# Kernel optimization log

Measured on AMD Instinct MI355X. Metric: run time of the kernel, lower is better.

The kernel has to match this reference:

```python
import jax, jax.numpy as jnp
import numpy as np

N, K, CONV_DIM = 100, 20, 256
TEMP, ALPHA = 0.1, 0.1
B_NORM = 1  # module hardcodes self.B = 1
BATCH = 8


def setup_inputs() -> dict:
    key = jax.random.key(0)
    inputs = jax.random.normal(key, (BATCH, N, K, CONV_DIM), dtype=jnp.float32)
    return {"inputs": inputs}


def reference(inputs) -> jnp.ndarray:
    # inputs: [B, N, K, D] prototype representations
    B, n, k, D = inputs.shape
    # L2-normalize along feature dim (reduce_euclidean_norm)
    xn = inputs / jnp.sqrt(jnp.sum(inputs * inputs, axis=-1, keepdims=True))
    flat = xn.reshape(B, n * k, D)  # all prototypes, all classes: [B, N*K, D]

    # anchor-vs-all similarities: [B, N, K, N*K]
    sims = jnp.einsum('bnkd,bmd->bnkm', xn, flat) / TEMP
    # anchor self-similarity (==1/t after normalization, but keep exact math): [B, N, K]
    self_sim = jnp.sum(xn * xn, axis=-1) / TEMP

    # denominator: sum_m exp(sim) - exp(self)
    denom = jnp.sum(jnp.exp(sims), axis=-1) - jnp.exp(self_sim)
    log_term = jnp.log(denom)  # [B, N, K]

    # intra-class similarity sum: anchor vs all K prototypes of its own class
    intra = jnp.einsum('bnkd,bnjd->bnk', xn, xn) / TEMP  # [B, N, K]
    sum_term = (intra - self_sim) / (k - 1)

    cl_loss = jnp.sum(log_term - sum_term)  # summed over batch and all N*K anchors
    loss = ALPHA * cl_loss / (B_NORM * n * k * D)
    return loss
```

## Files before the change

### kernel.cpp

```cpp
#include <hip/hip_runtime.h>
#include <math.h>

#define BB 8
#define NN 100
#define KK 20
#define DD 256
#define MM 2000
#define MP 2048
#define TINV 10.0f
#define LOSS_SCALE 1.953125e-7f

typedef __bf16 bf16x8 __attribute__((ext_vector_type(8)));
typedef float floatx4 __attribute__((ext_vector_type(4)));
typedef __attribute__((address_space(1))) const ushort GUshort;
typedef __attribute__((address_space(3))) ushort LUshort;

__device__ __forceinline__ ushort f2bf(float f) {
    unsigned int u = __float_as_uint(f);
    u += 0x7fffu + ((u >> 16) & 1u);
    return (ushort)(u >> 16);
}

__global__ void norm_bf16(const float* __restrict__ x, ushort* __restrict__ xb,
                          float* __restrict__ invn_out,
                          float* __restrict__ denom_g, float* __restrict__ out) {
    if (blockIdx.x < 16)
        ((float4*)denom_g)[blockIdx.x * 256 + threadIdx.x] = make_float4(0.f, 0.f, 0.f, 0.f);
    if (blockIdx.x == 0 && threadIdx.x == 0) out[0] = 0.0f;

    const int rg = blockIdx.x * 4 + (threadIdx.x >> 6);
    const int lane = threadIdx.x & 63;
    const int b = rg >> 11;
    const int r = rg & (MP - 1);
    ushort4 outv = make_ushort4(0, 0, 0, 0);
    if (r < MM) {
        const float4 v = ((const float4*)(x + ((size_t)(b * MM + r)) * DD))[lane];
        float s = v.x * v.x + v.y * v.y + v.z * v.z + v.w * v.w;
        #pragma unroll
        for (int o = 32; o >= 1; o >>= 1) s += __shfl_xor(s, o, 64);
        const float inv = 1.0f / sqrtf(s);
        if (lane == 0) invn_out[rg] = inv;
        outv.x = f2bf(v.x * inv);
        outv.y = f2bf(v.y * inv);
        outv.z = f2bf(v.z * inv);
        outv.w = f2bf(v.w * inv);
    }
    ((ushort4*)(xb + (size_t)rg * DD))[lane] = outv;
}

__global__ __launch_bounds__(256)
void cl_mfma(const ushort* __restrict__ xb, float* __restrict__ denom_g) {
    __shared__ __align__(16) ushort As[128 * 64];
    __shared__ __align__(16) ushort Bs[128 * 64];

    const int b = blockIdx.x & 7;
    const int ti = (blockIdx.x >> 3) & 15;
    const int tj = blockIdx.x >> 7;
    const int rbase = ti << 7;
    const int cbase = tj << 7;
    const ushort* __restrict__ xbb = xb + (size_t)b * MP * DD;

    const int tid = threadIdx.x;
    const int lane = tid & 63;
    const int w = tid >> 6;
    const int wr = (w >> 1) << 6;
    const int wc = (w & 1) << 6;
    const int tx = lane & 15;
    const int tx7 = tx & 7;
    const int quad = lane >> 4;

    const int srow = lane >> 3;
    const int sg = (lane & 7) ^ srow;

    floatx4 acc[4][4];
    #pragma unroll
    for (int mt = 0; mt < 4; ++mt)
        #pragma unroll
        for (int nt = 0; nt < 4; ++nt)
            acc[mt][nt] = (floatx4){0.f, 0.f, 0.f, 0.f};

    #pragma unroll 1
    for (int kc = 0; kc < 4; ++kc) {
        __syncthreads();
        #pragma unroll
        for (int q = 0; q < 4; ++q) {
            const int R = ((w << 2) + q) << 3;
            const size_t koff = (kc << 6) + (sg << 3);
            __builtin_amdgcn_global_load_lds(
                (GUshort*)(xbb + (size_t)(rbase + R + srow) * DD + koff),
                (LUshort*)(As + R * 64), 16, 0, 0);
            __builtin_amdgcn_global_load_lds(
                (GUshort*)(xbb + (size_t)(cbase + R + srow) * DD + koff),
                (LUshort*)(Bs + R * 64), 16, 0, 0);
        }
        __syncthreads();

        #pragma unroll
        for (int ks = 0; ks < 2; ++ks) {
            const int g = (ks << 2) + quad;
            const int gp = (g ^ tx7) << 3;
            bf16x8 af[4], bf[4];
            #pragma unroll
            for (int mt = 0; mt < 4; ++mt)
                af[mt] = *(const bf16x8*)(As + (wr + (mt << 4) + tx) * 64 + gp);
            #pragma unroll
            for (int nt = 0; nt < 4; ++nt)
                bf[nt] = *(const bf16x8*)(Bs + (wc + (nt << 4) + tx) * 64 + gp);
            #pragma unroll
            for (int mt = 0; mt < 4; ++mt)
                #pragma unroll
                for (int nt = 0; nt < 4; ++nt)
                    acc[mt][nt] = __builtin_amdgcn_mfma_f32_16x16x32_bf16(af[mt], bf[nt], acc[mt][nt], 0, 0, 0);
        }
    }

    int colv[4];
    bool colok[4];
    #pragma unroll
    for (int nt = 0; nt < 4; ++nt) {
        const int c = cbase + wc + (nt << 4) + tx;
        colv[nt] = c;
        colok[nt] = c < MM;
    }

    #pragma unroll
    for (int mt = 0; mt < 4; ++mt) {
        #pragma unroll
        for (int i = 0; i < 4; ++i) {
            const int row = rbase + wr + (mt << 4) + (quad << 2) + i;
            float de = 0.f;
            #pragma unroll
            for (int nt = 0; nt < 4; ++nt) {
                const float e = __expf(acc[mt][nt][i] * TINV);
                de += (colok[nt] && (colv[nt] != row)) ? e : 0.0f;
            }
            #pragma unroll
            for (int o = 8; o >= 1; o >>= 1)
                de += __shfl_xor(de, o, 64);
            if (tx == 0)
                atomicAdd(&denom_g[b * MP + row], de);
        }
    }
}

__global__ void finalize_combined(const float* __restrict__ x,
                                  const float* __restrict__ invn,
                                  const float* __restrict__ denom_g,
                                  float* __restrict__ out) {
    __shared__ float red[4];
    const int tid = threadIdx.x;
    if (blockIdx.x < 800) {
        const int g = blockIdx.x;
        const int b = g / NN;
        const int n = g - b * NN;
        const int row0 = n * KK;
        const float* __restrict__ xg = x + ((size_t)(b * MM + row0)) * DD;
        const float* __restrict__ ig = invn + b * MP + row0;
        float s = 0.0f;
        #pragma unroll
        for (int k = 0; k < KK; ++k)
            s = fmaf(ig[k], xg[(size_t)k * DD + tid], s);
        float v = s * s;
        #pragma unroll
        for (int o = 32; o >= 1; o >>= 1) v += __shfl_xor(v, o, 64);
        if ((tid & 63) == 0) red[tid >> 6] = v;
        __syncthreads();
        if (tid == 0) {
            const float S2 = red[0] + red[1] + red[2] + red[3];
            atomicAdd(out, -LOSS_SCALE * (TINV / (KK - 1)) * (S2 - (float)KK));
        }
    } else {
        const int i = (blockIdx.x - 800) * 256 + tid;
        float s = 0.0f;
        if (i < BB * MM) {
            const int b = i / MM;
            const int r = i - b * MM;
            s = logf(denom_g[b * MP + r]);
        }
        #pragma unroll
        for (int o = 32; o >= 1; o >>= 1) s += __shfl_xor(s, o, 64);
        if ((tid & 63) == 0) red[tid >> 6] = s;
        __syncthreads();
        if (tid == 0)
            atomicAdd(out, (red[0] + red[1] + red[2] + red[3]) * LOSS_SCALE);
    }
}

extern "C" void kernel_launch(void* const* d_in, const int* in_sizes, int n_in,
                              void* d_out, int out_size, void* d_ws, size_t ws_size,
                              hipStream_t stream) {
    const float* x = (const float*)d_in[0];
    float* out = (float*)d_out;
    float* denom_g = (float*)d_ws;
    float* invn = denom_g + BB * MP;
    ushort* xb = (ushort*)(invn + BB * MP);

    norm_bf16<<<BB * MP / 4, 256, 0, stream>>>(x, xb, invn, denom_g, out);
    cl_mfma<<<BB * 16 * 16, 256, 0, stream>>>(xb, denom_g);
    finalize_combined<<<800 + 63, 256, 0, stream>>>(x, invn, denom_g, out);
}
```

Before: 114.1 us.

## Load MFMA fragments directly from global memory with register double-buffering

Removes the LDS staging (global_load_lds plus barriers) from the similarity GEMM. Each wave now loads its bf16 A/B fragments straight from global memory into registers and prefetches the next K chunk while issuing MFMAs on the current one. This drops the syncthreads and LDS traffic, but the two wave pairs that share tile rows or columns now fetch the same data separately through L1/L2. It also uses more VGPRs for the double-buffered fragments, which may reduce occupancy.

```diff
diff --git a/kernel.cpp b/kernel.cpp
--- a/kernel.cpp
+++ b/kernel.cpp
@@ -12,8 +12,6 @@
 
 typedef __bf16 bf16x8 __attribute__((ext_vector_type(8)));
 typedef float floatx4 __attribute__((ext_vector_type(4)));
-typedef __attribute__((address_space(1))) const ushort GUshort;
-typedef __attribute__((address_space(3))) ushort LUshort;
 
 __device__ __forceinline__ ushort f2bf(float f) {
     unsigned int u = __float_as_uint(f);
@@ -50,27 +48,19 @@
 
 __global__ __launch_bounds__(256)
 void cl_mfma(const ushort* __restrict__ xb, float* __restrict__ denom_g) {
-    __shared__ __align__(16) ushort As[128 * 64];
-    __shared__ __align__(16) ushort Bs[128 * 64];
-
     const int b = blockIdx.x & 7;
     const int ti = (blockIdx.x >> 3) & 15;
     const int tj = blockIdx.x >> 7;
-    const int rbase = ti << 7;
-    const int cbase = tj << 7;
+    const int lane = threadIdx.x & 63;
+    const int w = threadIdx.x >> 6;
+    const int tx = lane & 15;
+    const int quad = lane >> 4;
+    const int rbase = (ti << 7) + ((w >> 1) << 6);
+    const int cbase = (tj << 7) + ((w & 1) << 6);
     const ushort* __restrict__ xbb = xb + (size_t)b * MP * DD;
 
-    const int tid = threadIdx.x;
-    const int lane = tid & 63;
-    const int w = tid >> 6;
-    const int wr = (w >> 1) << 6;
-    const int wc = (w & 1) << 6;
-    const int tx = lane & 15;
-    const int tx7 = tx & 7;
-    const int quad = lane >> 4;
-
-    const int srow = lane >> 3;
-    const int sg = (lane & 7) ^ srow;
+    const ushort* __restrict__ aRow = xbb + (size_t)(rbase + tx) * DD + (quad << 3);
+    const ushort* __restrict__ bRow = xbb + (size_t)(cbase + tx) * DD + (quad << 3);
 
     floatx4 acc[4][4];
     #pragma unroll
@@ -79,46 +69,45 @@
         for (int nt = 0; nt < 4; ++nt)
             acc[mt][nt] = (floatx4){0.f, 0.f, 0.f, 0.f};
 
-    #pragma unroll 1
-    for (int kc = 0; kc < 4; ++kc) {
-        __syncthreads();
-        #pragma unroll
-        for (int q = 0; q < 4; ++q) {
-            const int R = ((w << 2) + q) << 3;
-            const size_t koff = (kc << 6) + (sg << 3);
-            __builtin_amdgcn_global_load_lds(
-                (GUshort*)(xbb + (size_t)(rbase + R + srow) * DD + koff),
-                (LUshort*)(As + R * 64), 16, 0, 0);
-            __builtin_amdgcn_global_load_lds(
-                (GUshort*)(xbb + (size_t)(cbase + R + srow) * DD + koff),
-                (LUshort*)(Bs + R * 64), 16, 0, 0);
-        }
-        __syncthreads();
+    bf16x8 af[2][4][2], bfr[2][4][2];
 
+    #pragma unroll
+    for (int mt = 0; mt < 4; ++mt)
         #pragma unroll
         for (int ks = 0; ks < 2; ++ks) {
-            const int g = (ks << 2) + quad;
-            const int gp = (g ^ tx7) << 3;
-            bf16x8 af[4], bf[4];
+            af[0][mt][ks]  = *(const bf16x8*)(aRow + (size_t)(mt << 4) * DD + (ks << 5));
+            bfr[0][mt][ks] = *(const bf16x8*)(bRow + (size_t)(mt << 4) * DD + (ks << 5));
+        }
+
+    #pragma unroll
+    for (int kc = 0; kc < 4; ++kc) {
+        const int cur = kc & 1;
+        const int nxt = cur ^ 1;
+        if (kc < 3) {
+            const int ko = (kc + 1) << 6;
             #pragma unroll
             for (int mt = 0; mt < 4; ++mt)
-                af[mt] = *(const bf16x8*)(As + (wr + (mt << 4) + tx) * 64 + gp);
-            #pragma unroll
-            for (int nt = 0; nt < 4; ++nt)
-                bf[nt] = *(const bf16x8*)(Bs + (wc + (nt << 4) + tx) * 64 + gp);
+                #pragma unroll
+                for (int ks = 0; ks < 2; ++ks) {
+                    af[nxt][mt][ks]  = *(const bf16x8*)(aRow + (size_t)(mt << 4) * DD + ko + (ks << 5));
+                    bfr[nxt][mt][ks] = *(const bf16x8*)(bRow + (size_t)(mt << 4) * DD + ko + (ks << 5));
+                }
+        }
+        #pragma unroll
+        for (int ks = 0; ks < 2; ++ks)
             #pragma unroll
             for (int mt = 0; mt < 4; ++mt)
                 #pragma unroll
                 for (int nt = 0; nt < 4; ++nt)
-                    acc[mt][nt] = __builtin_amdgcn_mfma_f32_16x16x32_bf16(af[mt], bf[nt], acc[mt][nt], 0, 0, 0);
-        }
+                    acc[mt][nt] = __builtin_amdgcn_mfma_f32_16x16x32_bf16(
+                        af[cur][mt][ks], bfr[cur][nt][ks], acc[mt][nt], 0, 0, 0);
     }
 
     int colv[4];
     bool colok[4];
     #pragma unroll
     for (int nt = 0; nt < 4; ++nt) {
-        const int c = cbase + wc + (nt << 4) + tx;
+        const int c = cbase + (nt << 4) + tx;
         colv[nt] = c;
         colok[nt] = c < MM;
     }
@@ -127,7 +116,7 @@
     for (int mt = 0; mt < 4; ++mt) {
         #pragma unroll
         for (int i = 0; i < 4; ++i) {
-            const int row = rbase + wr + (mt << 4) + (quad << 2) + i;
+            const int row = rbase + (mt << 4) + (quad << 2) + i;
             float de = 0.f;
             #pragma unroll
             for (int nt = 0; nt < 4; ++nt) {
```

New measurement: 140.6 us. +23.3%, slower.
